# Kernel optimization log

Measured on AMD Instinct MI355X. Metric: run time of the kernel, lower is better.

Reference implementation:

```python
import jax, jax.numpy as jnp
import numpy as np

IN_DIM = 50400
OUT_DIM = 4096
SHARDS = 8
DIM_PER_SHARD = IN_DIM // SHARDS


def setup_inputs() -> dict:
    key = jax.random.key(0)
    k1, k2, k3 = jax.random.split(key, 3)
    x = jax.random.randint(k1, (8, 2048), 0, IN_DIM, dtype=jnp.int64 if jax.config.jax_enable_x64 else jnp.int32)
    # per-shard Linear weights: W[s] is [dim_per_shard, out_dim], TruncatedNormal(1/sqrt(in_dim))
    W = jax.random.normal(k2, (SHARDS, DIM_PER_SHARD, OUT_DIM), dtype=jnp.float32) / np.sqrt(IN_DIM)
    # per-shard Linear bias (haiku default init is zeros; random here to exercise the path)
    b = jax.random.normal(k3, (SHARDS, OUT_DIM), dtype=jnp.float32) * 0.01
    return {"x": x, "W": W, "b": b}


def reference(x, W, b):
    """Math of EmbeddingShard under pmean over 'shard':
    out = (1/S) * sum_s (onehot_s(x) @ W[s] + b[s])
    The one-hot matmul over each vocab shard is exactly a row-gather from the
    concatenated table, so we compute it as a gather (same math, efficient).
    """
    flat_x = x.reshape(-1)                      # [N]
    full_W = W.reshape(IN_Dim := IN_DIM, OUT_DIM)  # [in_dim, out_dim], shards concatenated along vocab
    gathered = jnp.take(full_W, flat_x, axis=0)    # [N, out_dim]
    bias_sum = b.sum(axis=0)                       # sum of per-shard biases
    return (gathered + bias_sum) / SHARDS          # pmean averaging
```

## Files before the change

kernel.cpp:

```cpp
#include <hip/hip_runtime.h>


#define IN_DIM   50400
#define OUT_DIM  4096
#define SHARDS   8
#define N_TOK    16384

__global__ __launch_bounds__(256) void bias_sum_kernel(const float* __restrict__ b,
                                                       float* __restrict__ bsum) {
    int j = blockIdx.x * blockDim.x + threadIdx.x;
    if (j < OUT_DIM) {
        float s = 0.0f;
#pragma unroll
        for (int sd = 0; sd < SHARDS; ++sd) {
            s += b[sd * OUT_DIM + j];
        }
        bsum[j] = s * (1.0f / SHARDS);
    }
}

__global__ __launch_bounds__(256) void gather_bias_kernel(const int* __restrict__ x,
                                                          const float* __restrict__ W,
                                                          const float* __restrict__ bsum,
                                                          float* __restrict__ out) {
    const int n = blockIdx.x;
    const int row = x[n];
    const float4* __restrict__ wrow = reinterpret_cast<const float4*>(W + (size_t)row * OUT_DIM);
    const float4* __restrict__ bs4  = reinterpret_cast<const float4*>(bsum);
    float4* __restrict__ orow       = reinterpret_cast<float4*>(out + (size_t)n * OUT_DIM);

#pragma unroll
    for (int i = 0; i < 4; ++i) {
        const int j = threadIdx.x + i * 256;
        const float4 w = wrow[j];
        const float4 bb = bs4[j];
        float4 o;
        o.x = fmaf(w.x, 0.125f, bb.x);
        o.y = fmaf(w.y, 0.125f, bb.y);
        o.z = fmaf(w.z, 0.125f, bb.z);
        o.w = fmaf(w.w, 0.125f, bb.w);
        orow[j] = o;
    }
}

extern "C" void kernel_launch(void* const* d_in, const int* in_sizes, int n_in,
                              void* d_out, int out_size, void* d_ws, size_t ws_size,
                              hipStream_t stream) {
    const int*   x = (const int*)d_in[0];
    const float* W = (const float*)d_in[1];
    const float* b = (const float*)d_in[2];
    float* out  = (float*)d_out;
    float* bsum = (float*)d_ws;

    bias_sum_kernel<<<(OUT_DIM + 255) / 256, 256, 0, stream>>>(b, bsum);
    gather_bias_kernel<<<N_TOK, 256, 0, stream>>>(x, W, bsum, out);
}
```

Before: 106.3 us.

## Use persistent grid-stride gather with nontemporal stores and hoisted bias

Replaces the one-block-per-token launch with a fixed grid of 2048 blocks. Each thread owns one float4 column and walks tokens with a stride, so the bias vector is loaded once per thread instead of once per element. Output writes use nontemporal stores to avoid polluting cache with the 256MB streaming output. The cost is fewer blocks in flight and per-iteration index loads, which may reduce memory-level parallelism.

```diff
diff --git a/kernel.cpp b/kernel.cpp
--- a/kernel.cpp
+++ b/kernel.cpp
@@ -6,40 +6,46 @@
 #define SHARDS   8
 #define N_TOK    16384
 
+#define BLOCKS   2048
+#define THREADS  256
+#define SLOTS4   (N_TOK * (OUT_DIM / 4))
+#define NTHREADS (BLOCKS * THREADS)
+#define ITERS    (SLOTS4 / NTHREADS)
+#define ROWSTEP  (NTHREADS / (OUT_DIM / 4))
+
+typedef float f4 __attribute__((ext_vector_type(4)));
+
 __global__ __launch_bounds__(256) void bias_sum_kernel(const float* __restrict__ b,
                                                        float* __restrict__ bsum) {
     int j = blockIdx.x * blockDim.x + threadIdx.x;
     if (j < OUT_DIM) {
         float s = 0.0f;
 #pragma unroll
-        for (int sd = 0; sd < SHARDS; ++sd) {
-            s += b[sd * OUT_DIM + j];
-        }
+        for (int sd = 0; sd < SHARDS; ++sd) s += b[sd * OUT_DIM + j];
         bsum[j] = s * (1.0f / SHARDS);
     }
 }
 
 __global__ __launch_bounds__(256) void gather_bias_kernel(const int* __restrict__ x,
-                                                          const float* __restrict__ W,
-                                                          const float* __restrict__ bsum,
-                                                          float* __restrict__ out) {
-    const int n = blockIdx.x;
-    const int row = x[n];
-    const float4* __restrict__ wrow = reinterpret_cast<const float4*>(W + (size_t)row * OUT_DIM);
-    const float4* __restrict__ bs4  = reinterpret_cast<const float4*>(bsum);
-    float4* __restrict__ orow       = reinterpret_cast<float4*>(out + (size_t)n * OUT_DIM);
+                                                          const f4* __restrict__ W4,
+                                                          const f4* __restrict__ bsum4,
+                                                          f4* __restrict__ out4) {
+    const int tid = blockIdx.x * THREADS + threadIdx.x;
+    const int j   = tid & (OUT_DIM / 4 - 1);
+    const int n0  = tid >> 10;
+    const f4 bb = bsum4[j];
 
-#pragma unroll
-    for (int i = 0; i < 4; ++i) {
-        const int j = threadIdx.x + i * 256;
-        const float4 w = wrow[j];
-        const float4 bb = bs4[j];
-        float4 o;
+#pragma unroll 4
+    for (int it = 0; it < ITERS; ++it) {
+        const int n   = n0 + it * ROWSTEP;
+        const int row = x[n];
+        const f4 w = W4[(size_t)row * (OUT_DIM / 4) + j];
+        f4 o;
         o.x = fmaf(w.x, 0.125f, bb.x);
         o.y = fmaf(w.y, 0.125f, bb.y);
         o.z = fmaf(w.z, 0.125f, bb.z);
         o.w = fmaf(w.w, 0.125f, bb.w);
-        orow[j] = o;
+        __builtin_nontemporal_store(o, &out4[(size_t)n * (OUT_DIM / 4) + j]);
     }
 }
 
@@ -53,5 +59,6 @@
     float* bsum = (float*)d_ws;
 
     bias_sum_kernel<<<(OUT_DIM + 255) / 256, 256, 0, stream>>>(b, bsum);
-    gather_bias_kernel<<<N_TOK, 256, 0, stream>>>(x, W, bsum, out);
+    gather_bias_kernel<<<BLOCKS, THREADS, 0, stream>>>(
+        x, (const f4*)W, (const f4*)bsum, (f4*)out);
 }
```

New measurement: 98.61 us. 7.2% less time.
